# Performance work log

Hardware: AMD Instinct MI355X
Metric: run time of the kernel (lower is better)

The kernel has to match this reference:

```python
import jax, jax.numpy as jnp
import numpy as np

HEADS = 8
DIM_HEAD = 64
SCALE = DIM_HEAD ** -0.5

def setup_inputs() -> dict:
    key = jax.random.key(0)
    ks = jax.random.split(key, 6)
    b, n, m, qd, cd = 4, 2048, 2048, 256, 256
    inner = HEADS * DIM_HEAD
    return {
        "x": jax.random.normal(ks[0], (b, n, qd), jnp.float32),
        "context": jax.random.normal(ks[1], (b, m, cd), jnp.float32),
        "Wq": jax.random.normal(ks[2], (inner, qd), jnp.float32) * 0.02,
        "bq": jnp.zeros((inner,), jnp.float32),
        "Wkv": jax.random.normal(ks[3], (2 * inner, cd), jnp.float32) * 0.02,
        "bkv": jnp.zeros((2 * inner,), jnp.float32),
        "Wo": jax.random.normal(ks[4], (qd, inner), jnp.float32) * 0.02,
        "bo": jnp.zeros((qd,), jnp.float32),
    }

def reference(x, context, Wq, bq, Wkv, bkv, Wo, bo):
    b, n, _ = x.shape
    m = context.shape[1]
    inner = HEADS * DIM_HEAD
    # 1x1 conv projections == pointwise linear
    q = jnp.einsum('bnd,ed->bne', x, Wq) + bq            # [b, n, inner]
    kv = jnp.einsum('bmd,ed->bme', context, Wkv) + bkv    # [b, m, 2*inner]
    k, v = kv[..., :inner], kv[..., inner:]
    q = q.reshape(b, n, HEADS, DIM_HEAD).transpose(0, 2, 1, 3)  # [b,h,n,d]
    k = k.reshape(b, m, HEADS, DIM_HEAD).transpose(0, 2, 1, 3)
    v = v.reshape(b, m, HEADS, DIM_HEAD).transpose(0, 2, 1, 3)
    sim = jnp.einsum('bhid,bhjd->bhij', q, k) * SCALE     # [b,h,n,m]
    attn = jax.nn.softmax(sim, axis=-1)
    out = jnp.einsum('bhij,bhjd->bhid', attn, v)          # [b,h,n,d]
    out = out.transpose(0, 2, 1, 3).reshape(b, n, inner)  # [b,n,inner]
    return jnp.einsum('bne,oe->bno', out, Wo) + bo        # [b,n,query_dim]
```

## Files before the change

kernel.cpp:

```cpp
#include <hip/hip_runtime.h>
#include <hip/hip_bf16.h>

#define NB 4
#define SEQ 2048
#define NHEADS 8
#define ROWS (NB * SEQ)

typedef __attribute__((ext_vector_type(8))) short bf16x8;
typedef __attribute__((ext_vector_type(4))) short bf16x4;
typedef __attribute__((ext_vector_type(4))) float f32x4;
typedef __attribute__((ext_vector_type(16))) float f32x16;

__device__ inline short f2bf(float x) {
    union { float f; unsigned u; } v; v.f = x;
    unsigned r = v.u + 0x7FFF + ((v.u >> 16) & 1);
    return (short)(r >> 16);
}

__device__ inline unsigned pack2bf(float a, float b) {
    __hip_bfloat162 h = __float22bfloat162_rn(make_float2(a, b));
    unsigned u; __builtin_memcpy(&u, &h, 4);
    return u;
}

__device__ inline bf16x8 pack8(float4 a, float4 b) {
    union { unsigned u[4]; bf16x8 v; } r;
    r.u[0] = pack2bf(a.x, a.y);
    r.u[1] = pack2bf(a.z, a.w);
    r.u[2] = pack2bf(b.x, b.y);
    r.u[3] = pack2bf(b.z, b.w);
    return r.v;
}

__device__ inline unsigned comb2(unsigned w1, unsigned w2, float inv) {
    union { unsigned v; float f; } a, b, c, d;
    a.v = w1 << 16;          b.v = w2 << 16;
    c.v = w1 & 0xffff0000u;  d.v = w2 & 0xffff0000u;
    return pack2bf((a.f + b.f) * inv, (c.f + d.f) * inv);
}

__global__ __launch_bounds__(256) void cvt_xc(
    const float* __restrict__ x, const float* __restrict__ ctx,
    short* __restrict__ xb, short* __restrict__ cb)
{
    const int i = blockIdx.x * 256 + threadIdx.x;
    const float* src; short* dst; int off;
    if (i < 524288) { src = x;   dst = xb; off = i; }
    else            { src = ctx; dst = cb; off = i - 524288; }
    const float4 v = ((const float4*)src)[off];
    uint2 o2;
    o2.x = pack2bf(v.x, v.y);
    o2.y = pack2bf(v.z, v.w);
    *(uint2*)(dst + (size_t)off * 4) = o2;
}

template <bool CVT_W>
__global__ __launch_bounds__(256) void gemm128(
    const short* __restrict__ A, const void* __restrict__ W_,
    const float* __restrict__ bias, short* __restrict__ out,
    int K, int Ccols, float scale)
{
    __shared__ short As[128 * 64];
    __shared__ short Ws[128 * 64];
    const int tid = threadIdx.x;
    const int w = tid >> 6, lane = tid & 63, low = lane & 15, quad = lane >> 4;
    const int wm = w >> 1, wn = w & 1;
    const int rM0 = blockIdx.y * 128, c0 = blockIdx.x * 128;
    const int srow = tid >> 3, sj = tid & 7;

    f32x4 acc[4][4];
#pragma unroll
    for (int mt = 0; mt < 4; ++mt)
#pragma unroll
        for (int nt = 0; nt < 4; ++nt) acc[mt][nt] = (f32x4){0.f, 0.f, 0.f, 0.f};

    float4 pwf[4][2];
    bf16x8 pab[4], pwb[4];

    auto loadA = [&](int c, int k0) {
        const int row = c * 32 + srow;
        pab[c] = *(const bf16x8*)(A + (size_t)(rM0 + row) * K + k0 + sj * 8);
    };
    auto loadW = [&](int c, int k0) {
        const int row = c * 32 + srow;
        if constexpr (CVT_W) {
            const float* p = (const float*)W_ + (size_t)(c0 + row) * K + k0 + sj * 8;
            pwf[c][0] = ((const float4*)p)[0];
            pwf[c][1] = ((const float4*)p)[1];
        } else {
            pwb[c] = *(const bf16x8*)((const short*)W_ + (size_t)(c0 + row) * K + k0 + sj * 8);
        }
    };

#pragma unroll
    for (int c = 0; c < 4; ++c) { loadA(c, 0); loadW(c, 0); }

    int k0 = 0;
    for (;;) {
        __syncthreads();
#pragma unroll
        for (int c = 0; c < 4; ++c) {
            const int row = c * 32 + srow;
            const int pc = sj ^ (row & 7);
            *(bf16x8*)(&As[row * 64 + pc * 8]) = pab[c];
            if constexpr (CVT_W) *(bf16x8*)(&Ws[row * 64 + pc * 8]) = pack8(pwf[c][0], pwf[c][1]);
            else                 *(bf16x8*)(&Ws[row * 64 + pc * 8]) = pwb[c];
        }
        __syncthreads();
        const int kn = k0 + 64;
        if (kn < K) {
#pragma unroll
            for (int c = 0; c < 4; ++c) { loadA(c, kn); loadW(c, kn); }
        }
#pragma unroll
        for (int kh = 0; kh < 2; ++kh) {
            bf16x8 af[4], bfv[4];
#pragma unroll
            for (int t = 0; t < 4; ++t) {
                const int ra = wm * 64 + t * 16 + low;
                af[t] = *(const bf16x8*)(&As[ra * 64 + ((kh * 4 + quad) ^ (ra & 7)) * 8]);
                const int rb = wn * 64 + t * 16 + low;
                bfv[t] = *(const bf16x8*)(&Ws[rb * 64 + ((kh * 4 + quad) ^ (rb & 7)) * 8]);
            }
#pragma unroll
            for (int mt = 0; mt < 4; ++mt)
#pragma unroll
                for (int nt = 0; nt < 4; ++nt)
                    acc[mt][nt] = __builtin_amdgcn_mfma_f32_16x16x32_bf16(af[mt], bfv[nt], acc[mt][nt], 0, 0, 0);
        }
        k0 = kn;
        if (k0 >= K) break;
    }

#pragma unroll
    for (int nt = 0; nt < 4; ++nt) {
        const int col = c0 + wn * 64 + nt * 16 + low;
        const float bv = bias[col];
#pragma unroll
        for (int mt = 0; mt < 4; ++mt) {
            const size_t rbase = (size_t)(rM0 + wm * 64 + mt * 16 + quad * 4);
#pragma unroll
            for (int r = 0; r < 4; ++r)
                out[(rbase + r) * Ccols + col] = f2bf((acc[mt][nt][r] + bv) * scale);
        }
    }
}

__global__ __launch_bounds__(256) void gemm64_q(
    const short* __restrict__ A, const float* __restrict__ W,
    const float* __restrict__ bias, short* __restrict__ out,
    int K, int Ccols, float scale)
{
    __shared__ short As[64 * 64];
    __shared__ short Ws[64 * 64];
    const int tid = threadIdx.x;
    const int w = tid >> 6, lane = tid & 63, low = lane & 15, quad = lane >> 4;
    const int wm = w >> 1, wn = w & 1;
    const int r0 = blockIdx.y * 64, c0 = blockIdx.x * 64;
    const int srow = tid >> 2;
    const int sc = (tid & 3) * 2;

    f32x4 acc[2][2];
#pragma unroll
    for (int mt = 0; mt < 2; ++mt)
#pragma unroll
        for (int nt = 0; nt < 2; ++nt) acc[mt][nt] = (f32x4){0.f, 0.f, 0.f, 0.f};

    bf16x8 pab[2];
    float4 pwf[2][2];

    auto loadA = [&](int k0) {
        const short* p = A + (size_t)(r0 + srow) * K + k0 + sc * 8;
        pab[0] = ((const bf16x8*)p)[0];
        pab[1] = ((const bf16x8*)p)[1];
    };
    auto loadW = [&](int k0) {
        const float* p = W + (size_t)(c0 + srow) * K + k0 + sc * 8;
        pwf[0][0] = ((const float4*)p)[0]; pwf[0][1] = ((const float4*)p)[1];
        pwf[1][0] = ((const float4*)p)[2]; pwf[1][1] = ((const float4*)p)[3];
    };

    loadA(0); loadW(0);

    int k0 = 0;
    for (;;) {
        __syncthreads();
#pragma unroll
        for (int c = 0; c < 2; ++c) {
            const int pc = (sc + c) ^ (srow & 7);
            *(bf16x8*)(&As[srow * 64 + pc * 8]) = pab[c];
            *(bf16x8*)(&Ws[srow * 64 + pc * 8]) = pack8(pwf[c][0], pwf[c][1]);
        }
        __syncthreads();
        const int kn = k0 + 64;
        if (kn < K) { loadA(kn); loadW(kn); }
#pragma unroll
        for (int kh = 0; kh < 2; ++kh) {
            bf16x8 af[2], bfv[2];
#pragma unroll
            for (int t = 0; t < 2; ++t) {
                const int ra = wm * 32 + t * 16 + low;
                af[t] = *(const bf16x8*)(&As[ra * 64 + ((kh * 4 + quad) ^ (ra & 7)) * 8]);
                const int rb = wn * 32 + t * 16 + low;
                bfv[t] = *(const bf16x8*)(&Ws[rb * 64 + ((kh * 4 + quad) ^ (rb & 7)) * 8]);
            }
#pragma unroll
            for (int mt = 0; mt < 2; ++mt)
#pragma unroll
                for (int nt = 0; nt < 2; ++nt)
                    acc[mt][nt] = __builtin_amdgcn_mfma_f32_16x16x32_bf16(af[mt], bfv[nt], acc[mt][nt], 0, 0, 0);
        }
        k0 = kn;
        if (k0 >= K) break;
    }

#pragma unroll
    for (int nt = 0; nt < 2; ++nt) {
        const int col = c0 + wn * 32 + nt * 16 + low;
        const float bv = bias[col];
#pragma unroll
        for (int mt = 0; mt < 2; ++mt) {
            const size_t rbase = (size_t)(r0 + wm * 32 + mt * 16 + quad * 4);
#pragma unroll
            for (int r = 0; r < 4; ++r)
                out[(rbase + r) * Ccols + col] = f2bf((acc[mt][nt][r] + bv) * scale);
        }
    }
}

__global__ __launch_bounds__(256) void gemm64_ocomb(
    const short* __restrict__ num, const float* __restrict__ lbuf,
    const float* __restrict__ W, const float* __restrict__ bias,
    float* __restrict__ out)
{
    const int K = 512, Ccols = 256;
    const size_t NHALF = (size_t)ROWS * 512;
    const int R8 = ROWS * 8;
    __shared__ short As[64 * 64];
    __shared__ short Ws[64 * 64];
    const int tid = threadIdx.x;
    const int w = tid >> 6, lane = tid & 63, low = lane & 15, quad = lane >> 4;
    const int wm = w >> 1, wn = w & 1;
    const int r0 = blockIdx.y * 64, c0 = blockIdx.x * 64;
    const int srow = tid >> 2;
    const int sc = (tid & 3) * 2;

    f32x4 acc[2][2];
#pragma unroll
    for (int mt = 0; mt < 2; ++mt)
#pragma unroll
        for (int nt = 0; nt < 2; ++nt) acc[mt][nt] = (f32x4){0.f, 0.f, 0.f, 0.f};

    uint4 pa1[2], pa2[2];
    float pinv;
    float4 pwf[2][2];

    auto loadA = [&](int k0) {
        const int hh = k0 >> 6;
        const int row = r0 + srow;
        pinv = lbuf[row * 8 + hh] + lbuf[R8 + row * 8 + hh];
        const short* p1 = num + (size_t)row * 512 + k0 + sc * 8;
        pa1[0] = ((const uint4*)p1)[0];
        pa1[1] = ((const uint4*)p1)[1];
        const short* p2 = p1 + NHALF;
        pa2[0] = ((const uint4*)p2)[0];
        pa2[1] = ((const uint4*)p2)[1];
    };
    auto loadW = [&](int k0) {
        const float* p = W + (size_t)(c0 + srow) * K + k0 + sc * 8;
        pwf[0][0] = ((const float4*)p)[0]; pwf[0][1] = ((const float4*)p)[1];
        pwf[1][0] = ((const float4*)p)[2]; pwf[1][1] = ((const float4*)p)[3];
    };

    loadA(0); loadW(0);

    int k0 = 0;
    for (;;) {
        __syncthreads();
        {
            const float inv = 1.f / pinv;
#pragma unroll
            for (int c = 0; c < 2; ++c) {
                const int pc = (sc + c) ^ (srow & 7);
                union { unsigned u[4]; bf16x8 v; } r;
                r.u[0] = comb2(pa1[c].x, pa2[c].x, inv);
                r.u[1] = comb2(pa1[c].y, pa2[c].y, inv);
                r.u[2] = comb2(pa1[c].z, pa2[c].z, inv);
                r.u[3] = comb2(pa1[c].w, pa2[c].w, inv);
                *(bf16x8*)(&As[srow * 64 + pc * 8]) = r.v;
                *(bf16x8*)(&Ws[srow * 64 + pc * 8]) = pack8(pwf[c][0], pwf[c][1]);
            }
        }
        __syncthreads();
        const int kn = k0 + 64;
        if (kn < K) { loadA(kn); loadW(kn); }
#pragma unroll
        for (int kh = 0; kh < 2; ++kh) {
            bf16x8 af[2], bfv[2];
#pragma unroll
            for (int t = 0; t < 2; ++t) {
                const int ra = wm * 32 + t * 16 + low;
                af[t] = *(const bf16x8*)(&As[ra * 64 + ((kh * 4 + quad) ^ (ra & 7)) * 8]);
                const int rb = wn * 32 + t * 16 + low;
                bfv[t] = *(const bf16x8*)(&Ws[rb * 64 + ((kh * 4 + quad) ^ (rb & 7)) * 8]);
            }
#pragma unroll
            for (int mt = 0; mt < 2; ++mt)
#pragma unroll
                for (int nt = 0; nt < 2; ++nt)
                    acc[mt][nt] = __builtin_amdgcn_mfma_f32_16x16x32_bf16(af[mt], bfv[nt], acc[mt][nt], 0, 0, 0);
        }
        k0 = kn;
        if (k0 >= K) break;
    }

#pragma unroll
    for (int nt = 0; nt < 2; ++nt) {
        const int col = c0 + wn * 32 + nt * 16 + low;
        const float bv = bias[col];
#pragma unroll
        for (int mt = 0; mt < 2; ++mt) {
            const size_t rbase = (size_t)(r0 + wm * 32 + mt * 16 + quad * 4);
#pragma unroll
            for (int r = 0; r < 4; ++r)
                out[(rbase + r) * Ccols + col] = acc[mt][nt][r] + bv;
        }
    }
}

#define KST 72
#define VST 72
#define PST 72

__global__ __launch_bounds__(256) void attn_mfma(
    const short* __restrict__ q2,
    const short* __restrict__ kv2,
    short* __restrict__ numb,
    float* __restrict__ lbuf)
{
    __shared__ short Ks[64 * KST];
    __shared__ short Vt[64 * VST];
    __shared__ short Ps[4][32 * PST];

    const int tid = threadIdx.x;
    const int w = tid >> 6;
    const int lane = tid & 63;
    const int l31 = lane & 31;
    const int h2 = lane >> 5;

    const int flat = blockIdx.x;
    const int h = flat & 7;
    const int rest = flat >> 3;
    const int half = rest & 1;
    const int rest2 = rest >> 1;
    const int qtile = rest2 & 15;
    const int b = rest2 >> 4;
    const int iq0 = qtile * 128;
    const int jt0 = half * 16;

    bf16x8 qr[4];
#pragma unroll
    for (int st = 0; st < 4; ++st)
        qr[st] = *(const bf16x8*)(q2 + (size_t)(b * SEQ + iq0 + w * 32 + l31) * 512
                                  + h * 64 + st * 16 + h2 * 8);

    const short* kbase = kv2 + (size_t)(b * SEQ) * 1024 + h * 64;
    const short* vbase = kbase + 512;
    short* pw = &Ps[w][0];

    float lsum = 0.f;
    f32x16 oacc[2];
#pragma unroll
    for (int dg = 0; dg < 2; ++dg)
#pragma unroll
        for (int r = 0; r < 16; ++r) oacc[dg][r] = 0.f;

    const int krow = tid >> 2;
    const int kc = (tid & 3) * 16;
    const int vk4 = (tid & 15) * 4;
    const int vd4 = (tid >> 4) * 4;

    bf16x8 pk0, pk1;
    bf16x4 pv0, pv1, pv2, pv3;
    {
        const short* ksrc = kbase + (size_t)(jt0 * 64 + krow) * 1024 + kc;
        pk0 = *(const bf16x8*)(ksrc);
        pk1 = *(const bf16x8*)(ksrc + 8);
        const short* vs = vbase + (size_t)(jt0 * 64 + vk4) * 1024 + vd4;
        pv0 = *(const bf16x4*)(vs);
        pv1 = *(const bf16x4*)(vs + 1024);
        pv2 = *(const bf16x4*)(vs + 2048);
        pv3 = *(const bf16x4*)(vs + 3072);
    }

    for (int jt = jt0; jt < jt0 + 16; ++jt) {
        __syncthreads();
        *(bf16x8*)(&Ks[krow * KST + kc]) = pk0;
        *(bf16x8*)(&Ks[krow * KST + kc + 8]) = pk1;
        {
            bf16x4 c0_, c1_, c2_, c3_;
            c0_[0] = pv0[0]; c0_[1] = pv1[0]; c0_[2] = pv2[0]; c0_[3] = pv3[0];
            c1_[0] = pv0[1]; c1_[1] = pv1[1]; c1_[2] = pv2[1]; c1_[3] = pv3[1];
            c2_[0] = pv0[2]; c2_[1] = pv1[2]; c2_[2] = pv2[2]; c2_[3] = pv3[2];
            c3_[0] = pv0[3]; c3_[1] = pv1[3]; c3_[2] = pv2[3]; c3_[3] = pv3[3];
            *(bf16x4*)(&Vt[(vd4 + 0) * VST + vk4]) = c0_;
            *(bf16x4*)(&Vt[(vd4 + 1) * VST + vk4]) = c1_;
            *(bf16x4*)(&Vt[(vd4 + 2) * VST + vk4]) = c2_;
            *(bf16x4*)(&Vt[(vd4 + 3) * VST + vk4]) = c3_;
        }
        __syncthreads();

        if (jt + 1 < jt0 + 16) {
            const short* ksrc = kbase + (size_t)((jt + 1) * 64 + krow) * 1024 + kc;
            pk0 = *(const bf16x8*)(ksrc);
            pk1 = *(const bf16x8*)(ksrc + 8);
            const short* vs = vbase + (size_t)((jt + 1) * 64 + vk4) * 1024 + vd4;
            pv0 = *(const bf16x4*)(vs);
            pv1 = *(const bf16x4*)(vs + 1024);
            pv2 = *(const bf16x4*)(vs + 2048);
            pv3 = *(const bf16x4*)(vs + 3072);
        }

#pragma unroll
        for (int kg = 0; kg < 2; ++kg) {
            f32x16 s;
#pragma unroll
            for (int r = 0; r < 16; ++r) s[r] = 0.f;
#pragma unroll
            for (int st = 0; st < 4; ++st) {
                const bf16x8 kf = *(const bf16x8*)(&Ks[(kg * 32 + l31) * KST + st * 16 + h2 * 8]);
                s = __builtin_amdgcn_mfma_f32_32x32x16_bf16(kf, qr[st], s, 0, 0, 0);
            }
#pragma unroll
            for (int g = 0; g < 4; ++g) {
                const float p0 = __builtin_amdgcn_exp2f(s[4 * g + 0]);
                const float p1 = __builtin_amdgcn_exp2f(s[4 * g + 1]);
                const float p2 = __builtin_amdgcn_exp2f(s[4 * g + 2]);
                const float p3 = __builtin_amdgcn_exp2f(s[4 * g + 3]);
                lsum += (p0 + p1) + (p2 + p3);
                uint2 u;
                u.x = pack2bf(p0, p1);
                u.y = pack2bf(p2, p3);
                *(uint2*)(&pw[l31 * PST + kg * 32 + 8 * g + 4 * h2]) = u;
            }
        }
        __builtin_amdgcn_wave_barrier();

#pragma unroll
        for (int st = 0; st < 4; ++st) {
            const bf16x8 pf = *(const bf16x8*)(&pw[l31 * PST + st * 16 + h2 * 8]);
#pragma unroll
            for (int dg = 0; dg < 2; ++dg) {
                const bf16x8 vf = *(const bf16x8*)(&Vt[(dg * 32 + l31) * VST + st * 16 + h2 * 8]);
                oacc[dg] = __builtin_amdgcn_mfma_f32_32x32x16_bf16(pf, vf, oacc[dg], 0, 0, 0);
            }
        }
        __builtin_amdgcn_wave_barrier();
    }

    lsum += __shfl_xor(lsum, 32);
    short* nb = numb + (size_t)half * ROWS * 512;
    float* lb = lbuf + (size_t)half * ROWS * 8;
    if (lane < 32)
        lb[(size_t)(b * SEQ + iq0 + w * 32 + l31) * 8 + h] = lsum;
#pragma unroll
    for (int dg = 0; dg < 2; ++dg)
#pragma unroll
        for (int r = 0; r < 16; ++r) {
            const int qrow = w * 32 + (r & 3) + 8 * (r >> 2) + 4 * h2;
            nb[(size_t)(b * SEQ + iq0 + qrow) * 512 + h * 64 + dg * 32 + l31] =
                f2bf(oacc[dg][r]);
        }
}

extern "C" void kernel_launch(void* const* d_in, const int* in_sizes, int n_in,
                              void* d_out, int out_size, void* d_ws, size_t ws_size,
                              hipStream_t stream) {
    const float* x   = (const float*)d_in[0];
    const float* ctx = (const float*)d_in[1];
    const float* Wq  = (const float*)d_in[2];
    const float* bq  = (const float*)d_in[3];
    const float* Wkv = (const float*)d_in[4];
    const float* bkv = (const float*)d_in[5];
    const float* Wo  = (const float*)d_in[6];
    const float* bo  = (const float*)d_in[7];
    float* out = (float*)d_out;

    short* xb   = (short*)d_ws;
    short* cb   = xb + (size_t)ROWS * 256;
    short* q2b  = cb + (size_t)ROWS * 256;
    short* kv2b = q2b + (size_t)ROWS * 512;
    short* numb = kv2b + (size_t)ROWS * 1024;
    float* lbuf = (float*)(numb + (size_t)2 * ROWS * 512);

    const float qscale = 0.125f * 1.44269504088896f;

    cvt_xc<<<4096, 256, 0, stream>>>(x, ctx, xb, cb);

    gemm64_q<<<dim3(512 / 64, ROWS / 64), 256, 0, stream>>>(
        xb, Wq, bq, q2b, 256, 512, qscale);
    gemm128<true><<<dim3(1024 / 128, ROWS / 128), 256, 0, stream>>>(
        cb, Wkv, bkv, kv2b, 256, 1024, 1.0f);
    attn_mfma<<<NB * NHEADS * (SEQ / 128) * 2, 256, 0, stream>>>(
        q2b, kv2b, numb, lbuf);
    gemm64_ocomb<<<dim3(256 / 64, ROWS / 64), 256, 0, stream>>>(
        numb, lbuf, Wo, bo, out);
}
```

Baseline: 169.8 us.

## Fuse Q projection into attention kernel prologue

Removes the separate x-to-bf16 conversion and the Q-projection GEMM. Each attention block now loads its 128 rows of x and the 64 rows of Wq for its head in fp32, converts them to bf16 in shared memory, and computes Q with MFMA before the attention loop. This drops two kernel launches and the global round-trip of the Q buffer. In exchange, Q is recomputed twice per head tile because of the split over two key halves, and the prologue adds extra loads and barriers to the attention kernel.

```diff
diff --git a/kernel.cpp b/kernel.cpp
--- a/kernel.cpp
+++ b/kernel.cpp
@@ -39,19 +39,15 @@
     return pack2bf((a.f + b.f) * inv, (c.f + d.f) * inv);
 }
 
-__global__ __launch_bounds__(256) void cvt_xc(
-    const float* __restrict__ x, const float* __restrict__ ctx,
-    short* __restrict__ xb, short* __restrict__ cb)
+__global__ __launch_bounds__(256) void cvt_c(
+    const float* __restrict__ ctx, short* __restrict__ cb)
 {
     const int i = blockIdx.x * 256 + threadIdx.x;
-    const float* src; short* dst; int off;
-    if (i < 524288) { src = x;   dst = xb; off = i; }
-    else            { src = ctx; dst = cb; off = i - 524288; }
-    const float4 v = ((const float4*)src)[off];
+    const float4 v = ((const float4*)ctx)[i];
     uint2 o2;
     o2.x = pack2bf(v.x, v.y);
     o2.y = pack2bf(v.z, v.w);
-    *(uint2*)(dst + (size_t)off * 4) = o2;
+    *(uint2*)(cb + (size_t)i * 4) = o2;
 }
 
 template <bool CVT_W>
@@ -139,88 +135,6 @@
 #pragma unroll
         for (int mt = 0; mt < 4; ++mt) {
             const size_t rbase = (size_t)(rM0 + wm * 64 + mt * 16 + quad * 4);
-#pragma unroll
-            for (int r = 0; r < 4; ++r)
-                out[(rbase + r) * Ccols + col] = f2bf((acc[mt][nt][r] + bv) * scale);
-        }
-    }
-}
-
-__global__ __launch_bounds__(256) void gemm64_q(
-    const short* __restrict__ A, const float* __restrict__ W,
-    const float* __restrict__ bias, short* __restrict__ out,
-    int K, int Ccols, float scale)
-{
-    __shared__ short As[64 * 64];
-    __shared__ short Ws[64 * 64];
-    const int tid = threadIdx.x;
-    const int w = tid >> 6, lane = tid & 63, low = lane & 15, quad = lane >> 4;
-    const int wm = w >> 1, wn = w & 1;
-    const int r0 = blockIdx.y * 64, c0 = blockIdx.x * 64;
-    const int srow = tid >> 2;
-    const int sc = (tid & 3) * 2;
-
-    f32x4 acc[2][2];
-#pragma unroll
-    for (int mt = 0; mt < 2; ++mt)
-#pragma unroll
-        for (int nt = 0; nt < 2; ++nt) acc[mt][nt] = (f32x4){0.f, 0.f, 0.f, 0.f};
-
-    bf16x8 pab[2];
-    float4 pwf[2][2];
-
-    auto loadA = [&](int k0) {
-        const short* p = A + (size_t)(r0 + srow) * K + k0 + sc * 8;
-        pab[0] = ((const bf16x8*)p)[0];
-        pab[1] = ((const bf16x8*)p)[1];
-    };
-    auto loadW = [&](int k0) {
-        const float* p = W + (size_t)(c0 + srow) * K + k0 + sc * 8;
-        pwf[0][0] = ((const float4*)p)[0]; pwf[0][1] = ((const float4*)p)[1];
-        pwf[1][0] = ((const float4*)p)[2]; pwf[1][1] = ((const float4*)p)[3];
-    };
-
-    loadA(0); loadW(0);
-
-    int k0 = 0;
-    for (;;) {
-        __syncthreads();
-#pragma unroll
-        for (int c = 0; c < 2; ++c) {
-            const int pc = (sc + c) ^ (srow & 7);
-            *(bf16x8*)(&As[srow * 64 + pc * 8]) = pab[c];
-            *(bf16x8*)(&Ws[srow * 64 + pc * 8]) = pack8(pwf[c][0], pwf[c][1]);
-        }
-        __syncthreads();
-        const int kn = k0 + 64;
-        if (kn < K) { loadA(kn); loadW(kn); }
-#pragma unroll
-        for (int kh = 0; kh < 2; ++kh) {
-            bf16x8 af[2], bfv[2];
-#pragma unroll
-            for (int t = 0; t < 2; ++t) {
-                const int ra = wm * 32 + t * 16 + low;
-                af[t] = *(const bf16x8*)(&As[ra * 64 + ((kh * 4 + quad) ^ (ra & 7)) * 8]);
-                const int rb = wn * 32 + t * 16 + low;
-                bfv[t] = *(const bf16x8*)(&Ws[rb * 64 + ((kh * 4 + quad) ^ (rb & 7)) * 8]);
-            }
-#pragma unroll
-            for (int mt = 0; mt < 2; ++mt)
-#pragma unroll
-                for (int nt = 0; nt < 2; ++nt)
-                    acc[mt][nt] = __builtin_amdgcn_mfma_f32_16x16x32_bf16(af[mt], bfv[nt], acc[mt][nt], 0, 0, 0);
-        }
-        k0 = kn;
-        if (k0 >= K) break;
-    }
-
-#pragma unroll
-    for (int nt = 0; nt < 2; ++nt) {
-        const int col = c0 + wn * 32 + nt * 16 + low;
-        const float bv = bias[col];
-#pragma unroll
-        for (int mt = 0; mt < 2; ++mt) {
-            const size_t rbase = (size_t)(r0 + wm * 32 + mt * 16 + quad * 4);
 #pragma unroll
             for (int r = 0; r < 4; ++r)
                 out[(rbase + r) * Ccols + col] = f2bf((acc[mt][nt][r] + bv) * scale);
@@ -333,7 +247,9 @@
 #define PST 72
 
 __global__ __launch_bounds__(256) void attn_mfma(
-    const short* __restrict__ q2,
+    const float* __restrict__ x,
+    const float* __restrict__ Wq,
+    const float* __restrict__ bq,
     const short* __restrict__ kv2,
     short* __restrict__ numb,
     float* __restrict__ lbuf)
@@ -358,11 +274,67 @@
     const int iq0 = qtile * 128;
     const int jt0 = half * 16;
 
+    const float qscale = 0.125f * 1.44269504088896f;
+
     bf16x8 qr[4];
-#pragma unroll
-    for (int st = 0; st < 4; ++st)
-        qr[st] = *(const bf16x8*)(q2 + (size_t)(b * SEQ + iq0 + w * 32 + l31) * 512
-                                  + h * 64 + st * 16 + h2 * 8);
+    {
+        short* xs = &Ps[0][0];
+        short* wqs = Ks;
+        f32x16 qacc[2];
+#pragma unroll
+        for (int dg = 0; dg < 2; ++dg)
+#pragma unroll
+            for (int r = 0; r < 16; ++r) qacc[dg][r] = 0.f;
+
+        const int xrow = tid >> 1;
+        const int xkc = (tid & 1) * 32;
+        const int wrow = tid >> 2;
+        const int wkc = (tid & 3) * 16;
+
+        for (int k0 = 0; k0 < 256; k0 += 64) {
+            __syncthreads();
+            {
+                const float* xp = x + (size_t)(b * SEQ + iq0 + xrow) * 256 + k0 + xkc;
+                *(bf16x8*)(&xs[xrow * PST + xkc])      = pack8(((const float4*)xp)[0], ((const float4*)xp)[1]);
+                *(bf16x8*)(&xs[xrow * PST + xkc + 8])  = pack8(((const float4*)xp)[2], ((const float4*)xp)[3]);
+                *(bf16x8*)(&xs[xrow * PST + xkc + 16]) = pack8(((const float4*)xp)[4], ((const float4*)xp)[5]);
+                *(bf16x8*)(&xs[xrow * PST + xkc + 24]) = pack8(((const float4*)xp)[6], ((const float4*)xp)[7]);
+                const float* wp = Wq + (size_t)(h * 64 + wrow) * 256 + k0 + wkc;
+                *(bf16x8*)(&wqs[wrow * KST + wkc])     = pack8(((const float4*)wp)[0], ((const float4*)wp)[1]);
+                *(bf16x8*)(&wqs[wrow * KST + wkc + 8]) = pack8(((const float4*)wp)[2], ((const float4*)wp)[3]);
+            }
+            __syncthreads();
+#pragma unroll
+            for (int st = 0; st < 4; ++st) {
+                const bf16x8 bx = *(const bf16x8*)(&xs[(w * 32 + l31) * PST + st * 16 + h2 * 8]);
+#pragma unroll
+                for (int dg = 0; dg < 2; ++dg) {
+                    const bf16x8 aw = *(const bf16x8*)(&wqs[(dg * 32 + l31) * KST + st * 16 + h2 * 8]);
+                    qacc[dg] = __builtin_amdgcn_mfma_f32_32x32x16_bf16(aw, bx, qacc[dg], 0, 0, 0);
+                }
+            }
+        }
+        __syncthreads();
+        short* Qs = &Ps[w][0];
+#pragma unroll
+        for (int dg = 0; dg < 2; ++dg)
+#pragma unroll
+            for (int g = 0; g < 4; ++g) {
+                const int d0 = dg * 32 + 8 * g + 4 * h2;
+                const float v0 = (qacc[dg][4 * g + 0] + bq[h * 64 + d0 + 0]) * qscale;
+                const float v1 = (qacc[dg][4 * g + 1] + bq[h * 64 + d0 + 1]) * qscale;
+                const float v2 = (qacc[dg][4 * g + 2] + bq[h * 64 + d0 + 2]) * qscale;
+                const float v3 = (qacc[dg][4 * g + 3] + bq[h * 64 + d0 + 3]) * qscale;
+                uint2 u;
+                u.x = pack2bf(v0, v1);
+                u.y = pack2bf(v2, v3);
+                *(uint2*)(&Qs[l31 * PST + d0]) = u;
+            }
+        __builtin_amdgcn_wave_barrier();
+#pragma unroll
+        for (int st = 0; st < 4; ++st)
+            qr[st] = *(const bf16x8*)(&Qs[l31 * PST + st * 16 + h2 * 8]);
+    }
 
     const short* kbase = kv2 + (size_t)(b * SEQ) * 1024 + h * 64;
     const short* vbase = kbase + 512;
@@ -486,23 +458,17 @@
     const float* bo  = (const float*)d_in[7];
     float* out = (float*)d_out;
 
-    short* xb   = (short*)d_ws;
-    short* cb   = xb + (size_t)ROWS * 256;
-    short* q2b  = cb + (size_t)ROWS * 256;
-    short* kv2b = q2b + (size_t)ROWS * 512;
+    short* cb   = (short*)d_ws;
+    short* kv2b = cb + (size_t)ROWS * 256;
     short* numb = kv2b + (size_t)ROWS * 1024;
     float* lbuf = (float*)(numb + (size_t)2 * ROWS * 512);
 
-    const float qscale = 0.125f * 1.44269504088896f;
-
-    cvt_xc<<<4096, 256, 0, stream>>>(x, ctx, xb, cb);
-
-    gemm64_q<<<dim3(512 / 64, ROWS / 64), 256, 0, stream>>>(
-        xb, Wq, bq, q2b, 256, 512, qscale);
+    cvt_c<<<2048, 256, 0, stream>>>(ctx, cb);
+
     gemm128<true><<<dim3(1024 / 128, ROWS / 128), 256, 0, stream>>>(
         cb, Wkv, bkv, kv2b, 256, 1024, 1.0f);
     attn_mfma<<<NB * NHEADS * (SEQ / 128) * 2, 256, 0, stream>>>(
-        q2b, kv2b, numb, lbuf);
+        x, Wq, bq, kv2b, numb, lbuf);
     gemm64_ocomb<<<dim3(256 / 64, ROWS / 64), 256, 0, stream>>>(
         numb, lbuf, Wo, bo, out);
 }
```

After: 180.8 us. 6.4% more time.

## Fuse input conversion and Q/KV projections into one fp32-reading kernel

Applied to the files above, without the earlier changes.

Removes the separate fp32-to-bf16 conversion kernel for x and context. The Q and KV projection GEMMs are merged into a single 64x64-tile launch that reads fp32 activations directly and converts them while staging into shared memory. This drops two launches and the round trip of the bf16 copies through global memory. In exchange, activation tiles are re-read as fp32 (twice the bytes) once per column tile, and the KV GEMM now uses smaller 64x64 tiles instead of 128x128, which lowers data reuse.

```diff
diff --git a/kernel.cpp b/kernel.cpp
--- a/kernel.cpp
+++ b/kernel.cpp
@@ -39,124 +39,32 @@
     return pack2bf((a.f + b.f) * inv, (c.f + d.f) * inv);
 }
 
-__global__ __launch_bounds__(256) void cvt_xc(
-    const float* __restrict__ x, const float* __restrict__ ctx,
-    short* __restrict__ xb, short* __restrict__ cb)
-{
-    const int i = blockIdx.x * 256 + threadIdx.x;
-    const float* src; short* dst; int off;
-    if (i < 524288) { src = x;   dst = xb; off = i; }
-    else            { src = ctx; dst = cb; off = i - 524288; }
-    const float4 v = ((const float4*)src)[off];
-    uint2 o2;
-    o2.x = pack2bf(v.x, v.y);
-    o2.y = pack2bf(v.z, v.w);
-    *(uint2*)(dst + (size_t)off * 4) = o2;
-}
-
-template <bool CVT_W>
-__global__ __launch_bounds__(256) void gemm128(
-    const short* __restrict__ A, const void* __restrict__ W_,
-    const float* __restrict__ bias, short* __restrict__ out,
-    int K, int Ccols, float scale)
-{
-    __shared__ short As[128 * 64];
-    __shared__ short Ws[128 * 64];
-    const int tid = threadIdx.x;
-    const int w = tid >> 6, lane = tid & 63, low = lane & 15, quad = lane >> 4;
-    const int wm = w >> 1, wn = w & 1;
-    const int rM0 = blockIdx.y * 128, c0 = blockIdx.x * 128;
-    const int srow = tid >> 3, sj = tid & 7;
-
-    f32x4 acc[4][4];
-#pragma unroll
-    for (int mt = 0; mt < 4; ++mt)
-#pragma unroll
-        for (int nt = 0; nt < 4; ++nt) acc[mt][nt] = (f32x4){0.f, 0.f, 0.f, 0.f};
-
-    float4 pwf[4][2];
-    bf16x8 pab[4], pwb[4];
-
-    auto loadA = [&](int c, int k0) {
-        const int row = c * 32 + srow;
-        pab[c] = *(const bf16x8*)(A + (size_t)(rM0 + row) * K + k0 + sj * 8);
-    };
-    auto loadW = [&](int c, int k0) {
-        const int row = c * 32 + srow;
-        if constexpr (CVT_W) {
-            const float* p = (const float*)W_ + (size_t)(c0 + row) * K + k0 + sj * 8;
-            pwf[c][0] = ((const float4*)p)[0];
-            pwf[c][1] = ((const float4*)p)[1];
-        } else {
-            pwb[c] = *(const bf16x8*)((const short*)W_ + (size_t)(c0 + row) * K + k0 + sj * 8);
-        }
-    };
-
-#pragma unroll
-    for (int c = 0; c < 4; ++c) { loadA(c, 0); loadW(c, 0); }
-
-    int k0 = 0;
-    for (;;) {
-        __syncthreads();
-#pragma unroll
-        for (int c = 0; c < 4; ++c) {
-            const int row = c * 32 + srow;
-            const int pc = sj ^ (row & 7);
-            *(bf16x8*)(&As[row * 64 + pc * 8]) = pab[c];
-            if constexpr (CVT_W) *(bf16x8*)(&Ws[row * 64 + pc * 8]) = pack8(pwf[c][0], pwf[c][1]);
-            else                 *(bf16x8*)(&Ws[row * 64 + pc * 8]) = pwb[c];
-        }
-        __syncthreads();
-        const int kn = k0 + 64;
-        if (kn < K) {
-#pragma unroll
-            for (int c = 0; c < 4; ++c) { loadA(c, kn); loadW(c, kn); }
-        }
-#pragma unroll
-        for (int kh = 0; kh < 2; ++kh) {
-            bf16x8 af[4], bfv[4];
-#pragma unroll
-            for (int t = 0; t < 4; ++t) {
-                const int ra = wm * 64 + t * 16 + low;
-                af[t] = *(const bf16x8*)(&As[ra * 64 + ((kh * 4 + quad) ^ (ra & 7)) * 8]);
-                const int rb = wn * 64 + t * 16 + low;
-                bfv[t] = *(const bf16x8*)(&Ws[rb * 64 + ((kh * 4 + quad) ^ (rb & 7)) * 8]);
-            }
-#pragma unroll
-            for (int mt = 0; mt < 4; ++mt)
-#pragma unroll
-                for (int nt = 0; nt < 4; ++nt)
-                    acc[mt][nt] = __builtin_amdgcn_mfma_f32_16x16x32_bf16(af[mt], bfv[nt], acc[mt][nt], 0, 0, 0);
-        }
-        k0 = kn;
-        if (k0 >= K) break;
-    }
-
-#pragma unroll
-    for (int nt = 0; nt < 4; ++nt) {
-        const int col = c0 + wn * 64 + nt * 16 + low;
-        const float bv = bias[col];
-#pragma unroll
-        for (int mt = 0; mt < 4; ++mt) {
-            const size_t rbase = (size_t)(rM0 + wm * 64 + mt * 16 + quad * 4);
-#pragma unroll
-            for (int r = 0; r < 4; ++r)
-                out[(rbase + r) * Ccols + col] = f2bf((acc[mt][nt][r] + bv) * scale);
-        }
-    }
-}
-
-__global__ __launch_bounds__(256) void gemm64_q(
-    const short* __restrict__ A, const float* __restrict__ W,
-    const float* __restrict__ bias, short* __restrict__ out,
-    int K, int Ccols, float scale)
+__global__ __launch_bounds__(256) void proj(
+    const float* __restrict__ x, const float* __restrict__ Wq,
+    const float* __restrict__ bq, const float* __restrict__ ctx,
+    const float* __restrict__ Wkv, const float* __restrict__ bkv,
+    short* __restrict__ q2b, short* __restrict__ kv2b, float qscale)
 {
     __shared__ short As[64 * 64];
     __shared__ short Ws[64 * 64];
     const int tid = threadIdx.x;
+    const int bid = blockIdx.x;
     const int w = tid >> 6, lane = tid & 63, low = lane & 15, quad = lane >> 4;
     const int wm = w >> 1, wn = w & 1;
-    const int r0 = blockIdx.y * 64, c0 = blockIdx.x * 64;
+    const int K = 256;
+
+    const float* A; const float* W; const float* bias;
+    short* outp; int Ccols; float scale; int u;
+    if (bid < 1024) {
+        u = bid; A = x; W = Wq; bias = bq; outp = q2b;
+        Ccols = 512; scale = qscale;
+    } else {
+        u = bid - 1024; A = ctx; W = Wkv; bias = bkv; outp = kv2b;
+        Ccols = 1024; scale = 1.0f;
+    }
+    const int c0 = (u >> 7) * 64;
+    const int r0 = (u & 127) * 64;
+
     const int srow = tid >> 2;
     const int sc = (tid & 3) * 2;
 
@@ -166,13 +74,11 @@
 #pragma unroll
         for (int nt = 0; nt < 2; ++nt) acc[mt][nt] = (f32x4){0.f, 0.f, 0.f, 0.f};
 
-    bf16x8 pab[2];
-    float4 pwf[2][2];
-
+    float4 paf[2][2], pwf[2][2];
     auto loadA = [&](int k0) {
-        const short* p = A + (size_t)(r0 + srow) * K + k0 + sc * 8;
-        pab[0] = ((const bf16x8*)p)[0];
-        pab[1] = ((const bf16x8*)p)[1];
+        const float* p = A + (size_t)(r0 + srow) * K + k0 + sc * 8;
+        paf[0][0] = ((const float4*)p)[0]; paf[0][1] = ((const float4*)p)[1];
+        paf[1][0] = ((const float4*)p)[2]; paf[1][1] = ((const float4*)p)[3];
     };
     auto loadW = [&](int k0) {
         const float* p = W + (size_t)(c0 + srow) * K + k0 + sc * 8;
@@ -188,7 +94,7 @@
 #pragma unroll
         for (int c = 0; c < 2; ++c) {
             const int pc = (sc + c) ^ (srow & 7);
-            *(bf16x8*)(&As[srow * 64 + pc * 8]) = pab[c];
+            *(bf16x8*)(&As[srow * 64 + pc * 8]) = pack8(paf[c][0], paf[c][1]);
             *(bf16x8*)(&Ws[srow * 64 + pc * 8]) = pack8(pwf[c][0], pwf[c][1]);
         }
         __syncthreads();
@@ -223,7 +129,7 @@
             const size_t rbase = (size_t)(r0 + wm * 32 + mt * 16 + quad * 4);
 #pragma unroll
             for (int r = 0; r < 4; ++r)
-                out[(rbase + r) * Ccols + col] = f2bf((acc[mt][nt][r] + bv) * scale);
+                outp[(rbase + r) * Ccols + col] = f2bf((acc[mt][nt][r] + bv) * scale);
         }
     }
 }
@@ -486,21 +392,14 @@
     const float* bo  = (const float*)d_in[7];
     float* out = (float*)d_out;
 
-    short* xb   = (short*)d_ws;
-    short* cb   = xb + (size_t)ROWS * 256;
-    short* q2b  = cb + (size_t)ROWS * 256;
+    short* q2b  = (short*)d_ws;
     short* kv2b = q2b + (size_t)ROWS * 512;
     short* numb = kv2b + (size_t)ROWS * 1024;
     float* lbuf = (float*)(numb + (size_t)2 * ROWS * 512);
 
     const float qscale = 0.125f * 1.44269504088896f;
 
-    cvt_xc<<<4096, 256, 0, stream>>>(x, ctx, xb, cb);
-
-    gemm64_q<<<dim3(512 / 64, ROWS / 64), 256, 0, stream>>>(
-        xb, Wq, bq, q2b, 256, 512, qscale);
-    gemm128<true><<<dim3(1024 / 128, ROWS / 128), 256, 0, stream>>>(
-        cb, Wkv, bkv, kv2b, 256, 1024, 1.0f);
+    proj<<<3072, 256, 0, stream>>>(x, Wq, bq, ctx, Wkv, bkv, q2b, kv2b, qscale);
     attn_mfma<<<NB * NHEADS * (SEQ / 128) * 2, 256, 0, stream>>>(
         q2b, kv2b, numb, lbuf);
     gemm64_ocomb<<<dim3(256 / 64, ROWS / 64), 256, 0, stream>>>(
```

Measured after the change: 172.2 us. About the same (+1.4%).
